# Performance work log

Hardware: AMD Instinct MI355X
Metric: run time of the kernel (lower is better)

Reference implementation:

```python
import jax, jax.numpy as jnp
import numpy as np

B, S, V, E, H, C = 64, 1024, 50000, 256, 256, 20
BOUND_P = 0.05  # ~20-word sentences


def setup_inputs() -> dict:
    key = jax.random.key(0)
    k1, k2, k3, k4, k5, k6, k7 = jax.random.split(key, 7)
    tokens = jax.random.randint(k1, (B, S), 2, V)
    is_bound = jax.random.uniform(k2, (B, S)) < BOUND_P
    batch_x = jnp.where(is_bound, 1, tokens)
    batch_x = batch_x.at[:, S - 1].set(1)  # force final sentence boundary
    batch_lens = jnp.full((B,), S, dtype=jnp.int32)
    emb = jax.random.normal(k3, (V, E), dtype=jnp.float32) * 0.1
    W1 = jax.random.normal(k4, (E, H), dtype=jnp.float32) * (1.0 / np.sqrt(E))
    b1 = jnp.zeros((H,), dtype=jnp.float32)
    W2 = jax.random.normal(k5, (H, H), dtype=jnp.float32) * (1.0 / np.sqrt(H))
    b2 = jnp.zeros((H,), dtype=jnp.float32)
    W3 = jax.random.normal(k6, (H, C), dtype=jnp.float32) * (1.0 / np.sqrt(H))
    b3 = jnp.zeros((C,), dtype=jnp.float32)
    return {"batch_x": batch_x, "batch_lens": batch_lens, "emb": emb,
            "W1": W1, "b1": b1, "W2": W2, "b2": b2, "W3": W3, "b3": b3}


def reference(batch_x, batch_lens, emb, W1, b1, W2, b2, W3, b3):
    # word embedding gather: (B,S,E)
    word_embed = emb[batch_x]
    # word2sent nn layer (position-wise fc + tanh), dropout=identity (eval)
    h = jnp.tanh(jnp.einsum('bse,eh->bsh', word_embed, W1) + b1)
    # sentence segmentation: token id 1 marks end of sentence (inclusive)
    is_bound = (batch_x == 1)
    bcum = jnp.cumsum(is_bound.astype(jnp.int32), axis=1)
    local_id = bcum - is_bound.astype(jnp.int32)  # sentence index of each token
    doc_lens = bcum[:, -1]                        # sentences per doc
    valid = local_id < doc_lens[:, None]          # tokens after last boundary dropped
    seg = jnp.arange(B, dtype=jnp.int32)[:, None] * S + local_id
    seg = jnp.where(valid, seg, B * S)            # dump invalid tokens in spare bucket
    h_flat = h.reshape(B * S, H)
    sums = jax.ops.segment_sum(h_flat, seg.reshape(-1), num_segments=B * S + 1)[:B * S]
    cnts = jax.ops.segment_sum(valid.astype(h.dtype).reshape(-1), seg.reshape(-1),
                               num_segments=B * S + 1)[:B * S]
    # word2sent mean pooling (padded/empty slots -> 0, matching F.pad)
    sent_embed = (sums / jnp.maximum(cnts, 1.0)[:, None]).reshape(B, S, H)
    # sent2doc nn layer + mean pooling over valid sentences
    sent_hidden = jnp.tanh(jnp.einsum('bsh,hk->bsk', sent_embed, W2) + b2)
    sent_valid = (jnp.arange(S)[None, :] < doc_lens[:, None]).astype(h.dtype)
    doc_embed = jnp.einsum('bsk,bs->bk', sent_hidden, sent_valid) / doc_lens[:, None].astype(h.dtype)
    # classifier head
    cat_space = doc_embed @ W3 + b3
    return jax.nn.log_softmax(cat_space, axis=-1)
```

## Files before the change

kernel.cpp:

```cpp
#include <hip/hip_runtime.h>
#include <hip/hip_bf16.h>
#include <cstdint>
#include <cstddef>

#define NB 64
#define NS 1024
#define NV 50000
#define NE 256
#define NH 256
#define NC 20
#define MAXSEG 25

typedef short bf16x8 __attribute__((ext_vector_type(8)));
typedef float f32x4 __attribute__((ext_vector_type(4)));

#define WS_W1T    0
#define WS_W2T    131072
#define WS_STARTS 262144
#define WS_LENS   524544
#define WS_PREF   524800
#define WS_PBLK   526848
#define WS_DSUM   13634048

__device__ inline float bf2f(unsigned short u) {
    return __uint_as_float(((unsigned int)u) << 16);
}
__device__ inline unsigned short f2bf(float f) {
    unsigned int x = __float_as_uint(f);
    unsigned int r = (x + 0x7FFFu + ((x >> 16) & 1u)) >> 16;
    return (unsigned short)r;
}
__device__ inline float fast_tanh(float x) {
    float e = __expf(2.f * x);
    return 1.f - 2.f / (e + 1.f);
}

__global__ void setup_kernel(const float* __restrict__ W1, const float* __restrict__ W2,
                             const int* __restrict__ x,
                             unsigned short* __restrict__ W1T, unsigned short* __restrict__ W2T,
                             int* __restrict__ starts, int* __restrict__ lens,
                             int* __restrict__ pref) {
    int blk = blockIdx.x;
    if (blk < 512) {
        int idx = blk * 256 + threadIdx.x;
        if (idx < NE * NH) {
            int h = idx >> 8, e = idx & 255;
            W1T[idx] = f2bf(W1[e * NH + h]);
        } else {
            int i = idx - NE * NH;
            int j = i >> 8, k = i & 255;
            W2T[i] = f2bf(W2[k * NH + j]);
        }
    } else {
        if (threadIdx.x >= 64) return;
        int b = blk - 512;
        int lane = threadIdx.x;
        const int* row = x + b * NS;
        int* st = starts + b * (NS + 1);
        if (lane == 0) st[0] = 0;
        int cnt = 0;
        for (int it = 0; it < NS / 64; ++it) {
            if ((it & 1) == 0 && lane == 0) pref[b * 8 + (it >> 1)] = cnt;
            int s = it * 64 + lane;
            bool isb = (row[s] == 1);
            unsigned long long bal = __ballot(isb);
            int pre = __popcll(bal & ((1ull << lane) - 1ull));
            if (isb) st[cnt + pre + 1] = s + 1;
            cnt += __popcll(bal);
        }
        if (lane == 0) lens[b] = cnt;
    }
}

__global__ __launch_bounds__(512, 4) void gemm1_kernel(
    const int* __restrict__ batch_x, const float* __restrict__ emb,
    const unsigned short* __restrict__ W1T, const float* __restrict__ b1,
    float* __restrict__ pblk)
{
    __shared__ unsigned short As[2][16][264];
    __shared__ unsigned short Hs[16][264];
    __shared__ int sidtab[128];

    int tid = threadIdx.x;
    int lane = tid & 63;
    int w = tid >> 6;
    int lr = lane & 15;
    int g = lane >> 4;
    int kb0 = g * 8;
    int base = blockIdx.x * 128;

    if (w == 0) {
        int cnt = 0;
        #pragma unroll
        for (int c = 0; c < 2; ++c) {
            int t = c * 64 + lane;
            bool isb = (batch_x[base + t] == 1);
            unsigned long long bal = __ballot(isb);
            int pre = __popcll(bal & ((1ull << lane) - 1ull));
            int sid = cnt + pre;
            sidtab[t] = sid < MAXSEG ? sid : MAXSEG - 1;
            cnt += __popcll(bal);
        }
    }

    bf16x8 Bf[16];
    #pragma unroll
    for (int ks = 0; ks < 8; ++ks)
        #pragma unroll
        for (int n = 0; n < 2; ++n)
            Bf[ks * 2 + n] = *reinterpret_cast<const bf16x8*>(
                W1T + (size_t)(w * 32 + n * 16 + lr) * NE + ks * 32 + kb0);
    float bb[2];
    #pragma unroll
    for (int n = 0; n < 2; ++n) bb[n] = b1[w * 32 + n * 16 + lr];

    float4 gr[2];
    #pragma unroll
    for (int i = 0; i < 2; ++i) {
        int f = tid + i * 512;
        int row = f >> 6, c4 = (f & 63) * 4;
        int xv = batch_x[base + row];
        gr[i] = *reinterpret_cast<const float4*>(emb + (size_t)xv * NE + c4);
    }
    #pragma unroll
    for (int i = 0; i < 2; ++i) {
        int f = tid + i * 512;
        int row = f >> 6, c4 = (f & 63) * 4;
        ushort4 u;
        u.x = f2bf(gr[i].x); u.y = f2bf(gr[i].y); u.z = f2bf(gr[i].z); u.w = f2bf(gr[i].w);
        *reinterpret_cast<ushort4*>(&As[0][row][c4]) = u;
    }

    int cur_sid = 0;
    float running = 0.f;

    for (int t = 0; t < 8; ++t) {
        __syncthreads();
        int cur = t & 1;

        if (t + 1 < 8) {
            #pragma unroll
            for (int i = 0; i < 2; ++i) {
                int f = tid + i * 512;
                int row = f >> 6, c4 = (f & 63) * 4;
                int xv = batch_x[base + (t + 1) * 16 + row];
                gr[i] = *reinterpret_cast<const float4*>(emb + (size_t)xv * NE + c4);
            }
        }

        f32x4 acc[2];
        #pragma unroll
        for (int n = 0; n < 2; ++n) acc[n] = (f32x4){0.f, 0.f, 0.f, 0.f};
        #pragma unroll
        for (int ks = 0; ks < 8; ++ks) {
            bf16x8 a = *reinterpret_cast<const bf16x8*>(&As[cur][lr][ks * 32 + kb0]);
            #pragma unroll
            for (int n = 0; n < 2; ++n)
                acc[n] = __builtin_amdgcn_mfma_f32_16x16x32_bf16(a, Bf[ks * 2 + n], acc[n], 0, 0, 0);
        }

        #pragma unroll
        for (int n = 0; n < 2; ++n) {
            int col = w * 32 + n * 16 + lr;
            #pragma unroll
            for (int j = 0; j < 4; ++j)
                Hs[g * 4 + j][col] = f2bf(fast_tanh(acc[n][j] + bb[n]));
        }
        __syncthreads();

        if (tid < 256) {
            int rowbase = t * 16;
            #pragma unroll
            for (int r = 0; r < 16; ++r) {
                int s = sidtab[rowbase + r];
                if (s != cur_sid) {
                    pblk[((size_t)blockIdx.x * MAXSEG + cur_sid) * NH + tid] = running;
                    running = 0.f; cur_sid = s;
                }
                running += bf2f(Hs[r][tid]);
            }
        }

        if (t + 1 < 8) {
            #pragma unroll
            for (int i = 0; i < 2; ++i) {
                int f = tid + i * 512;
                int row = f >> 6, c4 = (f & 63) * 4;
                ushort4 u;
                u.x = f2bf(gr[i].x); u.y = f2bf(gr[i].y); u.z = f2bf(gr[i].z); u.w = f2bf(gr[i].w);
                *reinterpret_cast<ushort4*>(&As[cur ^ 1][row][c4]) = u;
            }
        }
    }
    if (tid < 256)
        pblk[((size_t)blockIdx.x * MAXSEG + cur_sid) * NH + tid] = running;
}

__global__ __launch_bounds__(256, 2) void sgemm_kernel(
    const float* __restrict__ pblk, const int* __restrict__ starts,
    const int* __restrict__ lens, const int* __restrict__ pref,
    const unsigned short* __restrict__ W2T, const float* __restrict__ b2,
    float* __restrict__ dsum)
{
    int b = blockIdx.y;
    int t = blockIdx.x;
    int i0 = t * 16;
    int L = lens[b];
    if (i0 >= L) return;

    int tid = threadIdx.x;
    int lane = tid & 63;
    int w = tid >> 6;
    int lr = lane & 15;
    int g = lane >> 4;
    int kb0 = g * 8;

    __shared__ unsigned short ms[16][264];
    bf16x8 Bf[32];
    #pragma unroll
    for (int ks = 0; ks < 8; ++ks)
        #pragma unroll
        for (int n = 0; n < 4; ++n)
            Bf[ks * 4 + n] = *reinterpret_cast<const bf16x8*>(
                W2T + (size_t)(w * 64 + n * 16 + lr) * NH + ks * 32 + kb0);
    float bb[4];
    #pragma unroll
    for (int n = 0; n < 4; ++n) bb[n] = b2[w * 64 + n * 16 + lr];

    const int* st = starts + b * (NS + 1);
    for (int s = 0; s < 16; ++s) {
        int i = i0 + s;
        float m = 0.f;
        if (i < L) {
            int s0 = st[i], e0 = st[i + 1];
            int tb1 = (e0 - 1) >> 7;
            float sum = 0.f;
            for (int tb = s0 >> 7; tb <= tb1; ++tb) {
                int blk = b * 8 + tb;
                sum += pblk[((size_t)blk * MAXSEG + (i - pref[blk])) * NH + tid];
            }
            m = sum / (float)(e0 - s0);
        }
        ms[s][tid] = f2bf(m);
    }
    __syncthreads();

    f32x4 acc[4];
    #pragma unroll
    for (int n = 0; n < 4; ++n) acc[n] = (f32x4){0.f, 0.f, 0.f, 0.f};
    #pragma unroll
    for (int ks = 0; ks < 8; ++ks) {
        bf16x8 a = *reinterpret_cast<const bf16x8*>(&ms[lr][ks * 32 + kb0]);
        #pragma unroll
        for (int n = 0; n < 4; ++n)
            acc[n] = __builtin_amdgcn_mfma_f32_16x16x32_bf16(a, Bf[ks * 4 + n], acc[n], 0, 0, 0);
    }

    float* dp = dsum + ((size_t)b * 8 + t) * NH;
    #pragma unroll
    for (int n = 0; n < 4; ++n) {
        float v = 0.f;
        #pragma unroll
        for (int j = 0; j < 4; ++j) {
            int srow = i0 + g * 4 + j;
            float hv = tanhf(acc[n][j] + bb[n]);
            v += (srow < L) ? hv : 0.f;
        }
        v += __shfl_xor(v, 16, 64);
        v += __shfl_xor(v, 32, 64);
        if (g == 0) dp[w * 64 + n * 16 + lr] = v;
    }
}

__global__ __launch_bounds__(256) void doc_kernel(
    const float* __restrict__ dsum, const int* __restrict__ lens,
    const float* __restrict__ W3, const float* __restrict__ b3,
    float* __restrict__ out)
{
    int b = blockIdx.x;
    int j = threadIdx.x;
    int L = lens[b];
    int ntiles = (L + 15) >> 4;

    float s = 0.f;
    for (int t = 0; t < ntiles; ++t)
        s += dsum[((size_t)b * 8 + t) * NH + j];

    __shared__ float d[NH];
    d[j] = s / (float)L;
    __syncthreads();

    __shared__ float cat[NC];
    if (j < NC) {
        float a = b3[j];
        #pragma unroll 8
        for (int k = 0; k < NH; ++k) a += d[k] * W3[k * NC + j];
        cat[j] = a;
    }
    __syncthreads();

    if (j == 0) {
        float mx = -1e30f;
        for (int c = 0; c < NC; ++c) mx = fmaxf(mx, cat[c]);
        float se = 0.f;
        for (int c = 0; c < NC; ++c) se += expf(cat[c] - mx);
        float lse = logf(se) + mx;
        for (int c = 0; c < NC; ++c) out[b * NC + c] = cat[c] - lse;
    }
}

extern "C" void kernel_launch(void* const* d_in, const int* in_sizes, int n_in,
                              void* d_out, int out_size, void* d_ws, size_t ws_size,
                              hipStream_t stream) {
    const int*   batch_x = (const int*)d_in[0];
    const float* emb = (const float*)d_in[2];
    const float* W1  = (const float*)d_in[3];
    const float* b1  = (const float*)d_in[4];
    const float* W2  = (const float*)d_in[5];
    const float* b2  = (const float*)d_in[6];
    const float* W3  = (const float*)d_in[7];
    const float* b3  = (const float*)d_in[8];
    float* out = (float*)d_out;

    char* ws = (char*)d_ws;
    unsigned short* W1T   = (unsigned short*)(ws + WS_W1T);
    unsigned short* W2T   = (unsigned short*)(ws + WS_W2T);
    int*            starts= (int*)(ws + WS_STARTS);
    int*            lens  = (int*)(ws + WS_LENS);
    int*            pref  = (int*)(ws + WS_PREF);
    float*          pblk  = (float*)(ws + WS_PBLK);
    float*          dsum  = (float*)(ws + WS_DSUM);

    hipLaunchKernelGGL(setup_kernel, dim3(512 + NB), dim3(256), 0, stream,
                       W1, W2, batch_x, W1T, W2T, starts, lens, pref);
    hipLaunchKernelGGL(gemm1_kernel, dim3((NB * NS) / 128), dim3(512), 0, stream,
                       batch_x, emb, W1T, b1, pblk);
    hipLaunchKernelGGL(sgemm_kernel, dim3(8, NB), dim3(256), 0, stream,
                       pblk, starts, lens, pref, W2T, b2, dsum);
    hipLaunchKernelGGL(doc_kernel, dim3(NB), dim3(256), 0, stream,
                       dsum, lens, W3, b3, out);
}
```

Measured before the change: 72.47 us.

## Drop setup kernel; fuse weight conversion and segmentation into consumers, per-chunk pooling

Removes the setup kernel that converted W1/W2 to transposed bf16 and computed sentence starts and lengths. Each block now converts its own weight fragments from fp32 on load, and the sgemm and doc kernels rebuild the boundary scan from batch_x in shared memory. gemm1 no longer stages tanh outputs through shared memory with a serial running sum. It reduces each 16-row chunk's per-sentence partial sums with wave shuffles and writes them to a per-chunk buffer (MAXS=16 slots), so sgemm sums more, smaller partials. This saves a launch and a sync stage at the cost of redundant strided fp32 weight reads per block, redundant scans, and larger partial-sum traffic.

```diff
diff --git a/kernel.cpp b/kernel.cpp
--- a/kernel.cpp
+++ b/kernel.cpp
@@ -5,22 +5,16 @@
 
 #define NB 64
 #define NS 1024
-#define NV 50000
 #define NE 256
 #define NH 256
 #define NC 20
-#define MAXSEG 25
+#define MAXS 16
 
 typedef short bf16x8 __attribute__((ext_vector_type(8)));
 typedef float f32x4 __attribute__((ext_vector_type(4)));
 
-#define WS_W1T    0
-#define WS_W2T    131072
-#define WS_STARTS 262144
-#define WS_LENS   524544
-#define WS_PREF   524800
-#define WS_PBLK   526848
-#define WS_DSUM   13634048
+#define WS_PBLK 0
+#define WS_DSUM 67108864
 
 __device__ inline float bf2f(unsigned short u) {
     return __uint_as_float(((unsigned int)u) << 16);
@@ -35,50 +29,12 @@
     return 1.f - 2.f / (e + 1.f);
 }
 
-__global__ void setup_kernel(const float* __restrict__ W1, const float* __restrict__ W2,
-                             const int* __restrict__ x,
-                             unsigned short* __restrict__ W1T, unsigned short* __restrict__ W2T,
-                             int* __restrict__ starts, int* __restrict__ lens,
-                             int* __restrict__ pref) {
-    int blk = blockIdx.x;
-    if (blk < 512) {
-        int idx = blk * 256 + threadIdx.x;
-        if (idx < NE * NH) {
-            int h = idx >> 8, e = idx & 255;
-            W1T[idx] = f2bf(W1[e * NH + h]);
-        } else {
-            int i = idx - NE * NH;
-            int j = i >> 8, k = i & 255;
-            W2T[i] = f2bf(W2[k * NH + j]);
-        }
-    } else {
-        if (threadIdx.x >= 64) return;
-        int b = blk - 512;
-        int lane = threadIdx.x;
-        const int* row = x + b * NS;
-        int* st = starts + b * (NS + 1);
-        if (lane == 0) st[0] = 0;
-        int cnt = 0;
-        for (int it = 0; it < NS / 64; ++it) {
-            if ((it & 1) == 0 && lane == 0) pref[b * 8 + (it >> 1)] = cnt;
-            int s = it * 64 + lane;
-            bool isb = (row[s] == 1);
-            unsigned long long bal = __ballot(isb);
-            int pre = __popcll(bal & ((1ull << lane) - 1ull));
-            if (isb) st[cnt + pre + 1] = s + 1;
-            cnt += __popcll(bal);
-        }
-        if (lane == 0) lens[b] = cnt;
-    }
-}
-
 __global__ __launch_bounds__(512, 4) void gemm1_kernel(
     const int* __restrict__ batch_x, const float* __restrict__ emb,
-    const unsigned short* __restrict__ W1T, const float* __restrict__ b1,
+    const float* __restrict__ W1, const float* __restrict__ b1,
     float* __restrict__ pblk)
 {
     __shared__ unsigned short As[2][16][264];
-    __shared__ unsigned short Hs[16][264];
     __shared__ int sidtab[128];
 
     int tid = threadIdx.x;
@@ -97,19 +53,26 @@
             bool isb = (batch_x[base + t] == 1);
             unsigned long long bal = __ballot(isb);
             int pre = __popcll(bal & ((1ull << lane) - 1ull));
-            int sid = cnt + pre;
-            sidtab[t] = sid < MAXSEG ? sid : MAXSEG - 1;
+            sidtab[t] = cnt + pre;
             cnt += __popcll(bal);
         }
     }
 
     bf16x8 Bf[16];
     #pragma unroll
-    for (int ks = 0; ks < 8; ++ks)
-        #pragma unroll
-        for (int n = 0; n < 2; ++n)
-            Bf[ks * 2 + n] = *reinterpret_cast<const bf16x8*>(
-                W1T + (size_t)(w * 32 + n * 16 + lr) * NE + ks * 32 + kb0);
+    for (int ks = 0; ks < 8; ++ks) {
+        #pragma unroll
+        for (int n = 0; n < 2; ++n) {
+            int col = w * 32 + n * 16 + lr;
+            bf16x8 v;
+            #pragma unroll
+            for (int e = 0; e < 8; ++e) {
+                int k = ks * 32 + kb0 + e;
+                v[e] = (short)f2bf(W1[k * NH + col]);
+            }
+            Bf[ks * 2 + n] = v;
+        }
+    }
     float bb[2];
     #pragma unroll
     for (int n = 0; n < 2; ++n) bb[n] = b1[w * 32 + n * 16 + lr];
@@ -131,9 +94,6 @@
         *reinterpret_cast<ushort4*>(&As[0][row][c4]) = u;
     }
 
-    int cur_sid = 0;
-    float running = 0.f;
-
     for (int t = 0; t < 8; ++t) {
         __syncthreads();
         int cur = t & 1;
@@ -157,28 +117,6 @@
             #pragma unroll
             for (int n = 0; n < 2; ++n)
                 acc[n] = __builtin_amdgcn_mfma_f32_16x16x32_bf16(a, Bf[ks * 2 + n], acc[n], 0, 0, 0);
-        }
-
-        #pragma unroll
-        for (int n = 0; n < 2; ++n) {
-            int col = w * 32 + n * 16 + lr;
-            #pragma unroll
-            for (int j = 0; j < 4; ++j)
-                Hs[g * 4 + j][col] = f2bf(fast_tanh(acc[n][j] + bb[n]));
-        }
-        __syncthreads();
-
-        if (tid < 256) {
-            int rowbase = t * 16;
-            #pragma unroll
-            for (int r = 0; r < 16; ++r) {
-                int s = sidtab[rowbase + r];
-                if (s != cur_sid) {
-                    pblk[((size_t)blockIdx.x * MAXSEG + cur_sid) * NH + tid] = running;
-                    running = 0.f; cur_sid = s;
-                }
-                running += bf2f(Hs[r][tid]);
-            }
         }
 
         if (t + 1 < 8) {
@@ -191,23 +129,51 @@
                 *reinterpret_cast<ushort4*>(&As[cur ^ 1][row][c4]) = u;
             }
         }
-    }
-    if (tid < 256)
-        pblk[((size_t)blockIdx.x * MAXSEG + cur_sid) * NH + tid] = running;
+
+        float h[2][4];
+        #pragma unroll
+        for (int n = 0; n < 2; ++n)
+            #pragma unroll
+            for (int j = 0; j < 4; ++j)
+                h[n][j] = fast_tanh(acc[n][j] + bb[n]);
+
+        int tb = t * 16;
+        int sbase = sidtab[tb];
+        int nseg = sidtab[tb + 15] - sbase + 1;
+        int sid_[4];
+        #pragma unroll
+        for (int j = 0; j < 4; ++j) sid_[j] = sidtab[tb + g * 4 + j] - sbase;
+
+        size_t chunkoff = (size_t)(blockIdx.x * 8 + t) * (MAXS * NH);
+        for (int s = 0; s < nseg; ++s) {
+            #pragma unroll
+            for (int n = 0; n < 2; ++n) {
+                float v = 0.f;
+                #pragma unroll
+                for (int j = 0; j < 4; ++j)
+                    v += (sid_[j] == s) ? h[n][j] : 0.f;
+                v += __shfl_xor(v, 16, 64);
+                v += __shfl_xor(v, 32, 64);
+                if (g == 0)
+                    pblk[chunkoff + (size_t)s * NH + (w * 32 + n * 16 + lr)] = v;
+            }
+        }
+    }
 }
 
 __global__ __launch_bounds__(256, 2) void sgemm_kernel(
-    const float* __restrict__ pblk, const int* __restrict__ starts,
-    const int* __restrict__ lens, const int* __restrict__ pref,
-    const unsigned short* __restrict__ W2T, const float* __restrict__ b2,
+    const int* __restrict__ batch_x, const float* __restrict__ pblk,
+    const float* __restrict__ W2, const float* __restrict__ b2,
     float* __restrict__ dsum)
 {
+    __shared__ int st[NS + 1];
+    __shared__ int pref16[64];
+    __shared__ int L_sh;
+    __shared__ unsigned short ms[16][264];
+
     int b = blockIdx.y;
     int t = blockIdx.x;
     int i0 = t * 16;
-    int L = lens[b];
-    if (i0 >= L) return;
-
     int tid = threadIdx.x;
     int lane = tid & 63;
     int w = tid >> 6;
@@ -215,29 +181,55 @@
     int g = lane >> 4;
     int kb0 = g * 8;
 
-    __shared__ unsigned short ms[16][264];
+    if (w == 0) {
+        const int* row = batch_x + b * NS;
+        int cnt = 0;
+        if (lane == 0) st[0] = 0;
+        for (int it = 0; it < 16; ++it) {
+            bool isb = (row[it * 64 + lane] == 1);
+            unsigned long long bal = __ballot(isb);
+            if (lane < 4)
+                pref16[it * 4 + lane] = cnt + __popcll(bal & ((1ull << (16 * lane)) - 1ull));
+            int pre = __popcll(bal & ((1ull << lane) - 1ull));
+            if (isb) st[cnt + pre + 1] = it * 64 + lane + 1;
+            cnt += __popcll(bal);
+        }
+        if (lane == 0) L_sh = cnt;
+    }
+
     bf16x8 Bf[32];
     #pragma unroll
-    for (int ks = 0; ks < 8; ++ks)
-        #pragma unroll
-        for (int n = 0; n < 4; ++n)
-            Bf[ks * 4 + n] = *reinterpret_cast<const bf16x8*>(
-                W2T + (size_t)(w * 64 + n * 16 + lr) * NH + ks * 32 + kb0);
+    for (int ks = 0; ks < 8; ++ks) {
+        #pragma unroll
+        for (int n = 0; n < 4; ++n) {
+            int col = w * 64 + n * 16 + lr;
+            bf16x8 v;
+            #pragma unroll
+            for (int e = 0; e < 8; ++e) {
+                int k = ks * 32 + kb0 + e;
+                v[e] = (short)f2bf(W2[k * NH + col]);
+            }
+            Bf[ks * 4 + n] = v;
+        }
+    }
     float bb[4];
     #pragma unroll
     for (int n = 0; n < 4; ++n) bb[n] = b2[w * 64 + n * 16 + lr];
 
-    const int* st = starts + b * (NS + 1);
+    __syncthreads();
+    int L = L_sh;
+    if (i0 >= L) return;
+
     for (int s = 0; s < 16; ++s) {
         int i = i0 + s;
         float m = 0.f;
         if (i < L) {
             int s0 = st[i], e0 = st[i + 1];
-            int tb1 = (e0 - 1) >> 7;
             float sum = 0.f;
-            for (int tb = s0 >> 7; tb <= tb1; ++tb) {
-                int blk = b * 8 + tb;
-                sum += pblk[((size_t)blk * MAXSEG + (i - pref[blk])) * NH + tid];
+            int cb1 = (e0 - 1) >> 4;
+            for (int cb = s0 >> 4; cb <= cb1; ++cb) {
+                int rel = i - pref16[cb];
+                sum += pblk[((size_t)(b * 64 + cb) * MAXS + rel) * NH + tid];
             }
             m = sum / (float)(e0 - s0);
         }
@@ -273,24 +265,34 @@
 }
 
 __global__ __launch_bounds__(256) void doc_kernel(
-    const float* __restrict__ dsum, const int* __restrict__ lens,
+    const int* __restrict__ batch_x, const float* __restrict__ dsum,
     const float* __restrict__ W3, const float* __restrict__ b3,
     float* __restrict__ out)
 {
+    __shared__ int L_sh;
+    __shared__ float d[NH];
+    __shared__ float cat[NC];
+
     int b = blockIdx.x;
     int j = threadIdx.x;
-    int L = lens[b];
+
+    if (j < 64) {
+        const int* row = batch_x + b * NS;
+        int cnt = 0;
+        for (int it = 0; it < 16; ++it)
+            cnt += __popcll(__ballot(row[it * 64 + j] == 1));
+        if (j == 0) L_sh = cnt;
+    }
+    __syncthreads();
+    int L = L_sh;
     int ntiles = (L + 15) >> 4;
 
     float s = 0.f;
     for (int t = 0; t < ntiles; ++t)
         s += dsum[((size_t)b * 8 + t) * NH + j];
-
-    __shared__ float d[NH];
     d[j] = s / (float)L;
     __syncthreads();
 
-    __shared__ float cat[NC];
     if (j < NC) {
         float a = b3[j];
         #pragma unroll 8
@@ -323,20 +325,13 @@
     float* out = (float*)d_out;
 
     char* ws = (char*)d_ws;
-    unsigned short* W1T   = (unsigned short*)(ws + WS_W1T);
-    unsigned short* W2T   = (unsigned short*)(ws + WS_W2T);
-    int*            starts= (int*)(ws + WS_STARTS);
-    int*            lens  = (int*)(ws + WS_LENS);
-    int*            pref  = (int*)(ws + WS_PREF);
-    float*          pblk  = (float*)(ws + WS_PBLK);
-    float*          dsum  = (float*)(ws + WS_DSUM);
-
-    hipLaunchKernelGGL(setup_kernel, dim3(512 + NB), dim3(256), 0, stream,
-                       W1, W2, batch_x, W1T, W2T, starts, lens, pref);
+    float* pblk = (float*)(ws + WS_PBLK);
+    float* dsum = (float*)(ws + WS_DSUM);
+
     hipLaunchKernelGGL(gemm1_kernel, dim3((NB * NS) / 128), dim3(512), 0, stream,
-                       batch_x, emb, W1T, b1, pblk);
+                       batch_x, emb, W1, b1, pblk);
     hipLaunchKernelGGL(sgemm_kernel, dim3(8, NB), dim3(256), 0, stream,
-                       pblk, starts, lens, pref, W2T, b2, dsum);
+                       batch_x, pblk, W2, b2, dsum);
     hipLaunchKernelGGL(doc_kernel, dim3(NB), dim3(256), 0, stream,
-                       dsum, lens, W3, b3, out);
-}
+                       batch_x, dsum, W3, b3, out);
+}
```

Result: slower. 86.33 us (+19.1%).

## Reduce segment partial sums per 16-row chunk from MFMA registers

Applied to the files above, without the earlier changes.

Drops the LDS staging of tanh outputs and the serial per-column segmented scan in gemm1. Each wave now reduces its MFMA accumulator rows per sentence with cross-lane shuffles and writes partial sums per 16-token chunk. This removes one barrier per tile and the 256-thread serial loop. In exchange the partial-sum buffer is several times larger, there are more global writes and a finer-grained prefix table, and sgemm must sum more chunk partials per sentence. It also removes the MAXSEG clamp.

```diff
diff --git a/kernel.cpp b/kernel.cpp
--- a/kernel.cpp
+++ b/kernel.cpp
@@ -5,11 +5,10 @@
 
 #define NB 64
 #define NS 1024
-#define NV 50000
 #define NE 256
 #define NH 256
 #define NC 20
-#define MAXSEG 25
+#define MAXS 16
 
 typedef short bf16x8 __attribute__((ext_vector_type(8)));
 typedef float f32x4 __attribute__((ext_vector_type(4)));
@@ -18,9 +17,9 @@
 #define WS_W2T    131072
 #define WS_STARTS 262144
 #define WS_LENS   524544
-#define WS_PREF   524800
-#define WS_PBLK   526848
-#define WS_DSUM   13634048
+#define WS_PREF16 524800
+#define WS_PBLK   541184
+#define WS_DSUM   67650048
 
 __device__ inline float bf2f(unsigned short u) {
     return __uint_as_float(((unsigned int)u) << 16);
@@ -39,7 +38,7 @@
                              const int* __restrict__ x,
                              unsigned short* __restrict__ W1T, unsigned short* __restrict__ W2T,
                              int* __restrict__ starts, int* __restrict__ lens,
-                             int* __restrict__ pref) {
+                             int* __restrict__ pref16) {
     int blk = blockIdx.x;
     if (blk < 512) {
         int idx = blk * 256 + threadIdx.x;
@@ -59,11 +58,13 @@
         int* st = starts + b * (NS + 1);
         if (lane == 0) st[0] = 0;
         int cnt = 0;
-        for (int it = 0; it < NS / 64; ++it) {
-            if ((it & 1) == 0 && lane == 0) pref[b * 8 + (it >> 1)] = cnt;
+        for (int it = 0; it < 16; ++it) {
             int s = it * 64 + lane;
             bool isb = (row[s] == 1);
             unsigned long long bal = __ballot(isb);
+            if (lane < 4)
+                pref16[b * 64 + it * 4 + lane] =
+                    cnt + __popcll(bal & ((1ull << (16 * lane)) - 1ull));
             int pre = __popcll(bal & ((1ull << lane) - 1ull));
             if (isb) st[cnt + pre + 1] = s + 1;
             cnt += __popcll(bal);
@@ -78,7 +79,6 @@
     float* __restrict__ pblk)
 {
     __shared__ unsigned short As[2][16][264];
-    __shared__ unsigned short Hs[16][264];
     __shared__ int sidtab[128];
 
     int tid = threadIdx.x;
@@ -97,8 +97,7 @@
             bool isb = (batch_x[base + t] == 1);
             unsigned long long bal = __ballot(isb);
             int pre = __popcll(bal & ((1ull << lane) - 1ull));
-            int sid = cnt + pre;
-            sidtab[t] = sid < MAXSEG ? sid : MAXSEG - 1;
+            sidtab[t] = cnt + pre;
             cnt += __popcll(bal);
         }
     }
@@ -131,9 +130,6 @@
         *reinterpret_cast<ushort4*>(&As[0][row][c4]) = u;
     }
 
-    int cur_sid = 0;
-    float running = 0.f;
-
     for (int t = 0; t < 8; ++t) {
         __syncthreads();
         int cur = t & 1;
@@ -157,28 +153,6 @@
             #pragma unroll
             for (int n = 0; n < 2; ++n)
                 acc[n] = __builtin_amdgcn_mfma_f32_16x16x32_bf16(a, Bf[ks * 2 + n], acc[n], 0, 0, 0);
-        }
-
-        #pragma unroll
-        for (int n = 0; n < 2; ++n) {
-            int col = w * 32 + n * 16 + lr;
-            #pragma unroll
-            for (int j = 0; j < 4; ++j)
-                Hs[g * 4 + j][col] = f2bf(fast_tanh(acc[n][j] + bb[n]));
-        }
-        __syncthreads();
-
-        if (tid < 256) {
-            int rowbase = t * 16;
-            #pragma unroll
-            for (int r = 0; r < 16; ++r) {
-                int s = sidtab[rowbase + r];
-                if (s != cur_sid) {
-                    pblk[((size_t)blockIdx.x * MAXSEG + cur_sid) * NH + tid] = running;
-                    running = 0.f; cur_sid = s;
-                }
-                running += bf2f(Hs[r][tid]);
-            }
         }
 
         if (t + 1 < 8) {
@@ -191,14 +165,41 @@
                 *reinterpret_cast<ushort4*>(&As[cur ^ 1][row][c4]) = u;
             }
         }
-    }
-    if (tid < 256)
-        pblk[((size_t)blockIdx.x * MAXSEG + cur_sid) * NH + tid] = running;
+
+        float h[2][4];
+        #pragma unroll
+        for (int n = 0; n < 2; ++n)
+            #pragma unroll
+            for (int j = 0; j < 4; ++j)
+                h[n][j] = fast_tanh(acc[n][j] + bb[n]);
+
+        int tb = t * 16;
+        int sbase = sidtab[tb];
+        int nseg = sidtab[tb + 15] - sbase + 1;
+        int sid_[4];
+        #pragma unroll
+        for (int j = 0; j < 4; ++j) sid_[j] = sidtab[tb + g * 4 + j] - sbase;
+
+        size_t chunkoff = (size_t)(blockIdx.x * 8 + t) * (MAXS * NH);
+        for (int s = 0; s < nseg; ++s) {
+            #pragma unroll
+            for (int n = 0; n < 2; ++n) {
+                float v = 0.f;
+                #pragma unroll
+                for (int j = 0; j < 4; ++j)
+                    v += (sid_[j] == s) ? h[n][j] : 0.f;
+                v += __shfl_xor(v, 16, 64);
+                v += __shfl_xor(v, 32, 64);
+                if (g == 0)
+                    pblk[chunkoff + (size_t)s * NH + (w * 32 + n * 16 + lr)] = v;
+            }
+        }
+    }
 }
 
 __global__ __launch_bounds__(256, 2) void sgemm_kernel(
     const float* __restrict__ pblk, const int* __restrict__ starts,
-    const int* __restrict__ lens, const int* __restrict__ pref,
+    const int* __restrict__ lens, const int* __restrict__ pref16,
     const unsigned short* __restrict__ W2T, const float* __restrict__ b2,
     float* __restrict__ dsum)
 {
@@ -228,16 +229,17 @@
     for (int n = 0; n < 4; ++n) bb[n] = b2[w * 64 + n * 16 + lr];
 
     const int* st = starts + b * (NS + 1);
+    const int* pf = pref16 + b * 64;
     for (int s = 0; s < 16; ++s) {
         int i = i0 + s;
         float m = 0.f;
         if (i < L) {
             int s0 = st[i], e0 = st[i + 1];
-            int tb1 = (e0 - 1) >> 7;
             float sum = 0.f;
-            for (int tb = s0 >> 7; tb <= tb1; ++tb) {
-                int blk = b * 8 + tb;
-                sum += pblk[((size_t)blk * MAXSEG + (i - pref[blk])) * NH + tid];
+            int cb1 = (e0 - 1) >> 4;
+            for (int cb = s0 >> 4; cb <= cb1; ++cb) {
+                int rel = i - pf[cb];
+                sum += pblk[((size_t)(b * 64 + cb) * MAXS + rel) * NH + tid];
             }
             m = sum / (float)(e0 - s0);
         }
@@ -327,16 +329,16 @@
     unsigned short* W2T   = (unsigned short*)(ws + WS_W2T);
     int*            starts= (int*)(ws + WS_STARTS);
     int*            lens  = (int*)(ws + WS_LENS);
-    int*            pref  = (int*)(ws + WS_PREF);
+    int*            pref16= (int*)(ws + WS_PREF16);
     float*          pblk  = (float*)(ws + WS_PBLK);
     float*          dsum  = (float*)(ws + WS_DSUM);
 
     hipLaunchKernelGGL(setup_kernel, dim3(512 + NB), dim3(256), 0, stream,
-                       W1, W2, batch_x, W1T, W2T, starts, lens, pref);
+                       W1, W2, batch_x, W1T, W2T, starts, lens, pref16);
     hipLaunchKernelGGL(gemm1_kernel, dim3((NB * NS) / 128), dim3(512), 0, stream,
                        batch_x, emb, W1T, b1, pblk);
     hipLaunchKernelGGL(sgemm_kernel, dim3(8, NB), dim3(256), 0, stream,
-                       pblk, starts, lens, pref, W2T, b2, dsum);
+                       pblk, starts, lens, pref16, W2T, b2, dsum);
     hipLaunchKernelGGL(doc_kernel, dim3(NB), dim3(256), 0, stream,
                        dsum, lens, W3, b3, out);
 }
```

New measurement: 80.74 us. +11.4%, slower.
